# Kernel optimization log

Measured on AMD Instinct MI355X. Metric: run time of the kernel, lower is better.

Reference implementation:

```python
import jax, jax.numpy as jnp
import numpy as np

D_MODEL = 1024
H = 16
D_K = D_MODEL // H  # 64


def setup_inputs() -> dict:
    key = jax.random.key(0)
    ks = jax.random.split(key, 10)
    s = 1.0 / np.sqrt(D_MODEL)
    x = jax.random.normal(ks[0], (4, 2048, D_MODEL), dtype=jnp.float32)
    # Per-head linear weights stacked: [H, d_model, d_k]
    Wq = jax.random.uniform(ks[1], (H, D_MODEL, D_K), jnp.float32, -s, s)
    bq = jax.random.uniform(ks[2], (H, D_K), jnp.float32, -s, s)
    Wk = jax.random.uniform(ks[3], (H, D_MODEL, D_K), jnp.float32, -s, s)
    bk = jax.random.uniform(ks[4], (H, D_K), jnp.float32, -s, s)
    Wv = jax.random.uniform(ks[5], (H, D_MODEL, D_K), jnp.float32, -s, s)
    bv = jax.random.uniform(ks[6], (H, D_K), jnp.float32, -s, s)
    so = 1.0 / np.sqrt(H * D_K)
    Wo = jax.random.uniform(ks[7], (H * D_K, D_MODEL), jnp.float32, -so, so)
    bo = jax.random.uniform(ks[8], (D_MODEL,), jnp.float32, -so, so)
    return {"x": x, "Wq": Wq, "bq": bq, "Wk": Wk, "bk": bk, "Wv": Wv, "bv": bv, "Wo": Wo, "bo": bo}


def reference(x, Wq, bq, Wk, bk, Wv, bv, Wo, bo):
    # x: [B, S, D]; Wq/Wk/Wv: [H, D, d_k]; b*: [H, d_k]
    q = jnp.einsum('bsd,hdk->bhsk', x, Wq) + bq[None, :, None, :]
    k = jnp.einsum('bsd,hdk->bhsk', x, Wk) + bk[None, :, None, :]
    v = jnp.einsum('bsd,hdk->bhsk', x, Wv) + bv[None, :, None, :]
    scores = jnp.einsum('bhqk,bhsk->bhqs', q, k) / np.sqrt(D_K)
    S = x.shape[1]
    causal = jnp.triu(jnp.ones((S, S), dtype=bool), k=1)  # True above diagonal
    scores = jnp.where(causal, -jnp.inf, scores)
    attn = jax.nn.softmax(scores, axis=-1)
    ctx = jnp.einsum('bhqs,bhsk->bhqk', attn, v)  # [B, H, S, d_k]
    B = x.shape[0]
    # concat heads: torch cats head outputs along last dim -> [B, S, H*d_k]
    ctx = jnp.transpose(ctx, (0, 2, 1, 3)).reshape(B, S, H * D_K)
    return ctx @ Wo + bo
```

## Files before the change

kernel.cpp:

```cpp
#include <hip/hip_runtime.h>
#include <hip/hip_bf16.h>

typedef unsigned short u16;
typedef __attribute__((ext_vector_type(8))) short short8;
typedef __attribute__((ext_vector_type(4))) short short4v;
typedef __attribute__((ext_vector_type(4))) float floatx4;

#define D_MODEL 1024
#define NH 16
#define SEQ 2048
#define BATCH 4
#define M_ROWS 8192
#define N_QKV 3072
#define PS_LD 72

#define QSCALE 0.18033688011112042f
#define EXP2_OFF 11.541560327111707f

__device__ __forceinline__ u16 f2u(float f) {
    __hip_bfloat16 h = __float2bfloat16(f);
    u16 u; __builtin_memcpy(&u, &h, 2); return u;
}

__device__ __forceinline__ void async_copy16(const u16* g, u16* l) {
    __builtin_amdgcn_global_load_lds(
        (const __attribute__((address_space(1))) unsigned int*)(g),
        (__attribute__((address_space(3))) unsigned int*)(l),
        16, 0, 0);
}

__global__ __launch_bounds__(256) void prep(
    const float* __restrict__ x,
    const float* __restrict__ Wq, const float* __restrict__ Wk,
    const float* __restrict__ Wv, const float* __restrict__ Wo,
    const float* __restrict__ bq, const float* __restrict__ bk,
    const float* __restrict__ bv, const float* __restrict__ bo,
    u16* __restrict__ xb, u16* __restrict__ Wpt, u16* __restrict__ Wot,
    float* __restrict__ biasp)
{
    __shared__ u16 T[64 * 72];
    const int tid = threadIdx.x;
    const int blk = blockIdx.x;

    if (blk < 4096) {
        size_t i = ((size_t)blk * 256 + tid) * 8;
        float4 f0 = *(const float4*)&x[i];
        float4 f1 = *(const float4*)&x[i + 4];
        u16 t[8] = {f2u(f0.x), f2u(f0.y), f2u(f0.z), f2u(f0.w),
                    f2u(f1.x), f2u(f1.y), f2u(f1.z), f2u(f1.w)};
        *(short8*)&xb[i] = *(short8*)t;
        return;
    }
    if (blk == 5120) {
        #pragma unroll
        for (int j = 0; j < 16; j++) {
            int idx = j * 256 + tid;
            float v;
            if (idx < 1024)      v = bq[idx] * QSCALE;
            else if (idx < 2048) v = bk[idx - 1024];
            else if (idx < 3072) v = bv[idx - 2048];
            else                 v = bo[idx - 3072];
            biasp[idx] = v;
        }
        return;
    }
    const int wb = blk - 4096;
    const int r = tid >> 2, s4 = (tid & 3) * 16;
    if (wb < 768) {
        int sel = wb / 256, rem = wb % 256;
        int h = rem >> 4, ktile = rem & 15;
        const float* W = (sel == 0) ? Wq : ((sel == 1) ? Wk : Wv);
        const float scale = (sel == 0) ? QSCALE : 1.0f;
        const float* src = W + ((size_t)h * 1024 + ktile * 64 + r) * 64 + s4;
        #pragma unroll
        for (int i = 0; i < 16; i++) T[(s4 + i) * 72 + r] = f2u(src[i] * scale);
        __syncthreads();
        u16 tmp[16];
        #pragma unroll
        for (int i = 0; i < 16; i++) tmp[i] = T[r * 72 + s4 + i];
        u16* dst = Wpt + ((size_t)sel * 1024 + h * 64 + r) * 1024 + ktile * 64 + s4;
        *(short8*)&dst[0] = *(short8*)&tmp[0];
        *(short8*)&dst[8] = *(short8*)&tmp[8];
    } else {
        int rem = wb - 768;
        int nt = rem >> 4, kt2 = rem & 15;
        const float* src = Wo + ((size_t)kt2 * 64 + r) * 1024 + nt * 64 + s4;
        #pragma unroll
        for (int i = 0; i < 16; i++) T[(s4 + i) * 72 + r] = f2u(src[i]);
        __syncthreads();
        u16 tmp[16];
        #pragma unroll
        for (int i = 0; i < 16; i++) tmp[i] = T[r * 72 + s4 + i];
        u16* dst = Wot + ((size_t)nt * 64 + r) * 1024 + kt2 * 64 + s4;
        *(short8*)&dst[0] = *(short8*)&tmp[0];
        *(short8*)&dst[8] = *(short8*)&tmp[8];
    }
}

__global__ __launch_bounds__(256) void vtrans(const u16* __restrict__ QKV,
                                              u16* __restrict__ Vtg) {
    __shared__ u16 T[64 * 72];
    const int bh = blockIdx.x, kt = blockIdx.y;
    const int b = bh >> 4, h = bh & 15;
    const int tid = threadIdx.x;
    const int r = tid >> 2, s4 = (tid & 3) * 16;
    const u16* vp = QKV + (size_t)(b * SEQ + kt * 64 + r) * N_QKV + 2 * D_MODEL + h * 64 + s4;
    *(short8*)&T[r * 72 + s4]     = *(const short8*)&vp[0];
    *(short8*)&T[r * 72 + s4 + 8] = *(const short8*)&vp[8];
    __syncthreads();
    u16 tmp[16];
    #pragma unroll
    for (int i = 0; i < 16; i++) tmp[i] = T[(s4 + i) * 72 + r];
    u16* op = Vtg + ((size_t)bh * 64 + r) * SEQ + kt * 64 + s4;
    *(short8*)&op[0] = *(short8*)&tmp[0];
    *(short8*)&op[8] = *(short8*)&tmp[8];
}

template <typename OT>
__global__ __launch_bounds__(256) void gemm128(
    const u16* __restrict__ A, const u16* __restrict__ Bt,
    const float* __restrict__ bias, OT* __restrict__ C,
    int M, int N, int K)
{
    __shared__ u16 As[128 * 64];
    __shared__ u16 Bs[128 * 64];
    const int tid = threadIdx.x;
    const int w = tid >> 6, lane = tid & 63;
    const int l16 = lane & 15, quad = lane >> 4;

    const int nwgx = gridDim.x;
    const int nwg = nwgx * gridDim.y;
    const int lin = blockIdx.y * nwgx + blockIdx.x;
    const int cpx = nwg >> 3;
    const int swz = (lin & 7) * cpx + (lin >> 3);
    const int bn = (swz % nwgx) * 128, bm = (swz / nwgx) * 128;

    const int wr = (w >> 1) * 64, wc = (w & 1) * 64;

    floatx4 acc[4][4];
    #pragma unroll
    for (int i = 0; i < 4; i++)
        #pragma unroll
        for (int j = 0; j < 4; j++) acc[i][j] = (floatx4){0.f, 0.f, 0.f, 0.f};

    for (int k0 = 0; k0 < K; k0 += 64) {
        #pragma unroll
        for (int c = 0; c < 4; c++) {
            const int off = (w * 4 + c) * 1024 + lane * 16;
            const int row = off >> 7, seg = (off >> 4) & 7;
            async_copy16(A  + (size_t)(bm + row) * K + k0 + seg * 8, &As[(w * 4 + c) * 512]);
            async_copy16(Bt + (size_t)(bn + row) * K + k0 + seg * 8, &Bs[(w * 4 + c) * 512]);
        }
        __syncthreads();
        #pragma unroll
        for (int kc = 0; kc < 2; kc++) {
            short8 a[4], b[4];
            #pragma unroll
            for (int i = 0; i < 4; i++)
                a[i] = *(short8*)&As[(wr + i * 16 + l16) * 64 + kc * 32 + quad * 8];
            #pragma unroll
            for (int i = 0; i < 4; i++)
                b[i] = *(short8*)&Bs[(wc + i * 16 + l16) * 64 + kc * 32 + quad * 8];
            #pragma unroll
            for (int mm = 0; mm < 4; mm++)
                #pragma unroll
                for (int nn = 0; nn < 4; nn++)
                    acc[mm][nn] = __builtin_amdgcn_mfma_f32_16x16x32_bf16(
                        a[mm], b[nn], acc[mm][nn], 0, 0, 0);
        }
        __syncthreads();
    }

    #pragma unroll
    for (int nn = 0; nn < 4; nn++) {
        const int col = bn + wc + nn * 16 + l16;
        const float bi = bias[col];
        #pragma unroll
        for (int mm = 0; mm < 4; mm++) {
            const int row = bm + wr + mm * 16 + quad * 4;
            #pragma unroll
            for (int r = 0; r < 4; r++) {
                float v = acc[mm][nn][r] + bi;
                if constexpr (sizeof(OT) == 2) ((u16*)C)[(size_t)(row + r) * N + col] = f2u(v);
                else                           C[(size_t)(row + r) * N + col] = v;
            }
        }
    }
}

#define G256_BAR   __builtin_amdgcn_s_barrier()
#define G256_LGKM0 { asm volatile("s_waitcnt lgkmcnt(0)" ::: "memory"); \
                     __builtin_amdgcn_sched_barrier(0); }

#define G256_STG(dstbase, s0, s1) { \
    async_copy16((s0), &lds[(dstbase) + stw]); \
    async_copy16((s1), &lds[(dstbase) + 4096 + stw]); }

#define G256_STAGE_A(bb, half, kq) \
    G256_STG((bb) * 32768 + (half) * 8192, \
             pA[0] + (size_t)(half) * hstep + (kq), \
             pA[1] + (size_t)(half) * hstep + (kq))

#define G256_STAGE_B(bb, half, kq) \
    G256_STG((bb) * 32768 + 16384 + (half) * 8192, \
             pB[0] + (size_t)(half) * hstep + (kq), \
             pB[1] + (size_t)(half) * hstep + (kq))

#define G256_LDA4(dst, bb, mi0) { \
    const int _b = (bb) * 32768 + wm * 8192; \
    _Pragma("unroll") \
    for (int mi = 0; mi < 4; mi++) { \
        const int _r = _b + (((mi0) + mi) * 16 + l16) * 64; \
        dst[mi * 2]     = *(const short8*)&lds[_r + col0]; \
        dst[mi * 2 + 1] = *(const short8*)&lds[_r + col1]; \
    } }

#define G256_LDB2(dst, bb, ni0) { \
    const int _b = (bb) * 32768 + 16384 + (wn >> 1) * 8192 + (wn & 1) * 4096; \
    _Pragma("unroll") \
    for (int ni = 0; ni < 2; ni++) { \
        const int _r = _b + (((ni0) + ni) * 16 + l16) * 64; \
        dst[ni * 2]     = *(const short8*)&lds[_r + col0]; \
        dst[ni * 2 + 1] = *(const short8*)&lds[_r + col1]; \
    } }

#define G256_MMA8(av, bv, MI0, NI0) { \
    _Pragma("unroll") \
    for (int mi = 0; mi < 4; mi++) \
    _Pragma("unroll") \
    for (int ni = 0; ni < 2; ni++) { \
        acc[(MI0) + mi][(NI0) + ni] = __builtin_amdgcn_mfma_f32_16x16x32_bf16( \
            bv[ni * 2],     av[mi * 2],     acc[(MI0) + mi][(NI0) + ni], 0, 0, 0); \
        acc[(MI0) + mi][(NI0) + ni] = __builtin_amdgcn_mfma_f32_16x16x32_bf16( \
            bv[ni * 2 + 1], av[mi * 2 + 1], acc[(MI0) + mi][(NI0) + ni], 0, 0, 0); \
    } }

template <typename OT>
__global__ __launch_bounds__(512, 2) void gemm256(
    const u16* __restrict__ A, const u16* __restrict__ Bt,
    const float* __restrict__ bias, OT* __restrict__ C,
    int M, int N, int K)
{
    __shared__ u16 lds[65536];
    const int tid = threadIdx.x;
    const int w = tid >> 6, lane = tid & 63;
    const int l16 = lane & 15, quad = lane >> 4;
    const int wm = w >> 2, wn = w & 3;

    const int nwgx = gridDim.x;
    const int nwg = nwgx * gridDim.y;
    const int lin = blockIdx.y * nwgx + blockIdx.x;
    const int cpx = nwg >> 3;
    const int swz = (lin & 7) * cpx + (lin >> 3);
    const int bn = (swz % nwgx) * 256, bm = (swz / nwgx) * 256;

    const u16* pA[2]; const u16* pB[2];
    #pragma unroll
    for (int j = 0; j < 2; j++) {
        const int d = (j * 512 + tid) * 16;
        const int s = d ^ (((d >> 7) & 7) << 4);
        const int r = s >> 7;
        const int c = (s & 127) >> 1;
        pA[j] = A  + (size_t)(bm + r) * K + c;
        pB[j] = Bt + (size_t)(bn + r) * K + c;
    }
    const size_t hstep = (size_t)128 * K;
    const int stw = w * 512;

    const int xm = (l16 & 7) << 3;
    const int col0 = (quad * 8) ^ xm;
    const int col1 = (32 + quad * 8) ^ xm;

    floatx4 acc[8][4];
    #pragma unroll
    for (int i = 0; i < 8; i++)
        #pragma unroll
        for (int j = 0; j < 4; j++) acc[i][j] = (floatx4){0.f, 0.f, 0.f, 0.f};

    G256_STAGE_A(0, 0, 0);  G256_STAGE_A(0, 1, 0);
    G256_STAGE_B(0, 0, 0);  G256_STAGE_B(0, 1, 0);
    G256_STAGE_B(1, 0, 64); G256_STAGE_B(1, 1, 64);
    G256_STAGE_A(1, 0, 64);
    asm volatile("s_waitcnt vmcnt(6)" ::: "memory");
    __syncthreads();

    short8 aL[8], aH[8], bL[4], bH[4];
    const int NKT = K >> 6;
    for (int kt = 0; kt < NKT; ++kt) {
        const int buf = kt & 1, nb = buf ^ 1;
        const int kqA = (kt + 1) << 6, kqB = (kt + 2) << 6;
        const bool st1 = (kt + 1 < NKT), st2 = (kt + 2 < NKT);

        G256_LDA4(aL, buf, 0);
        G256_LDB2(bL, buf, 0);
        if (st1) { G256_STAGE_A(nb, 1, kqA); }
        asm volatile("s_waitcnt lgkmcnt(8)" ::: "memory");
        G256_BAR; G256_LGKM0;
        __builtin_amdgcn_s_setprio(1); G256_MMA8(aL, bL, 0, 0);
        __builtin_amdgcn_s_setprio(0); G256_BAR;

        G256_LDB2(bH, buf, 2);
        G256_BAR; G256_LGKM0;
        __builtin_amdgcn_s_setprio(1); G256_MMA8(aL, bH, 0, 2);
        __builtin_amdgcn_s_setprio(0); G256_BAR;

        G256_LDA4(aH, buf, 4);
        if (st2) { G256_STAGE_B(buf, 0, kqB); }
        G256_BAR; G256_LGKM0;
        __builtin_amdgcn_s_setprio(1); G256_MMA8(aH, bH, 4, 2);
        __builtin_amdgcn_s_setprio(0); G256_BAR;

        if (st2) { G256_STAGE_B(buf, 1, kqB); G256_STAGE_A(buf, 0, kqB); }
        __builtin_amdgcn_s_setprio(1); G256_MMA8(aH, bL, 4, 0);
        __builtin_amdgcn_s_setprio(0);
        __builtin_amdgcn_sched_barrier(0);
        if (st2)      { asm volatile("s_waitcnt vmcnt(6)" ::: "memory"); }
        else if (st1) { asm volatile("s_waitcnt vmcnt(0)" ::: "memory"); }
        G256_BAR;
    }

    float4 bi[4];
    #pragma unroll
    for (int ni = 0; ni < 4; ni++)
        bi[ni] = *(const float4*)&bias[bn + wn * 64 + ni * 16 + quad * 4];
    #pragma unroll
    for (int mi = 0; mi < 8; mi++) {
        const int row = bm + wm * 128 + mi * 16 + l16;
        #pragma unroll
        for (int ni = 0; ni < 4; ni++) {
            const int col = bn + wn * 64 + ni * 16 + quad * 4;
            const float v0 = acc[mi][ni][0] + bi[ni].x;
            const float v1 = acc[mi][ni][1] + bi[ni].y;
            const float v2 = acc[mi][ni][2] + bi[ni].z;
            const float v3 = acc[mi][ni][3] + bi[ni].w;
            if constexpr (sizeof(OT) == 2) {
                u16 o[4] = {f2u(v0), f2u(v1), f2u(v2), f2u(v3)};
                *(short4v*)&((u16*)C)[(size_t)row * N + col] = *(short4v*)o;
            } else {
                float4 fv = {v0, v1, v2, v3};
                *(float4*)&C[(size_t)row * N + col] = fv;
            }
        }
    }
}

__global__ __launch_bounds__(256) void attn_mfma(
    const u16* __restrict__ QKV, const u16* __restrict__ Vtg, u16* __restrict__ ctx)
{
    __shared__ u16 Ks[2][64 * 64];
    __shared__ u16 Vs[2][64 * 64];
    __shared__ u16 Ps[128 * PS_LD];

    const int bh = blockIdx.x;
    const int qt = (int)(gridDim.y - 1) - (int)blockIdx.y;
    const int b = bh >> 4, h = bh & 15;
    const int tid = threadIdx.x;
    const int w = tid >> 6, lane = tid & 63;
    const int l16 = lane & 15, quad = lane >> 4;

    const int r0 = tid >> 3,        c0 = tid & 7;
    const int r1 = (256 + tid) >> 3, c1 = tid & 7;
    const int sw0 = c0 ^ (r0 & 7), sw1 = c1 ^ (r1 & 7);

    short8 q[2][2];
    #pragma unroll
    for (int m = 0; m < 2; m++) {
        const u16* qp = QKV + (size_t)(b * SEQ + qt * 128 + w * 32 + m * 16 + l16) * N_QKV + h * 64;
        q[m][0] = *(const short8*)&qp[quad * 8];
        q[m][1] = *(const short8*)&qp[32 + quad * 8];
    }

    short8 ones8;
    #pragma unroll
    for (int i = 0; i < 8; i++) ones8[i] = (short)0x3F80;

    floatx4 O[2][4];
    floatx4 lsum[2];
    #pragma unroll
    for (int m = 0; m < 2; m++) {
        lsum[m] = (floatx4){0.f, 0.f, 0.f, 0.f};
        #pragma unroll
        for (int i = 0; i < 4; i++) O[m][i] = (floatx4){0.f, 0.f, 0.f, 0.f};
    }

    const int nkt = 2 * qt + 2;
    const int qrow_w_max = qt * 128 + w * 32 + 31;

    const size_t kbase = (size_t)(b * SEQ) * N_QKV + D_MODEL + h * 64;
    const size_t vbase = (size_t)bh * 64 * SEQ;

    const u16* kpa = QKV + kbase + (size_t)r0 * N_QKV + c0 * 8;
    const u16* kpb = QKV + kbase + (size_t)r1 * N_QKV + c1 * 8;
    const u16* vpa = Vtg + vbase + (size_t)r0 * SEQ + c0 * 8;
    const u16* vpb = Vtg + vbase + (size_t)r1 * SEQ + c1 * 8;

    {
        float4 ka = *(const float4*)kpa;
        float4 kb = *(const float4*)kpb;
        float4 va = *(const float4*)vpa;
        float4 vb = *(const float4*)vpb;
        *(float4*)&Ks[0][r0 * 64 + sw0 * 8] = ka;
        *(float4*)&Ks[0][r1 * 64 + sw1 * 8] = kb;
        *(float4*)&Vs[0][r0 * 64 + sw0 * 8] = va;
        *(float4*)&Vs[0][r1 * 64 + sw1 * 8] = vb;
    }
    kpa += (size_t)64 * N_QKV; kpb += (size_t)64 * N_QKV;
    vpa += 64; vpb += 64;
    __syncthreads();

    for (int kt = 0; kt < nkt; kt++) {
        const int buf = kt & 1;
        const bool pre = (kt + 1 < nkt);
        float4 ka, kb, va, vb;
        if (pre) {
            ka = *(const float4*)kpa;
            kb = *(const float4*)kpb;
            va = *(const float4*)vpa;
            vb = *(const float4*)vpb;
            kpa += (size_t)64 * N_QKV; kpb += (size_t)64 * N_QKV;
            vpa += 64; vpb += 64;
        }

        if (kt * 64 <= qrow_w_max) {
            short8 kf[4][2];
            #pragma unroll
            for (int ns = 0; ns < 4; ns++) {
                const int rr = ns * 16 + l16, rs = rr & 7;
                kf[ns][0] = *(short8*)&Ks[buf][rr * 64 + (quad ^ rs) * 8];
                kf[ns][1] = *(short8*)&Ks[buf][rr * 64 + ((4 + quad) ^ rs) * 8];
            }
            const bool needMask = (kt * 64 + 63 > qt * 128 + w * 32);

            #pragma unroll
            for (int m = 0; m < 2; m++) {
                floatx4 z[4];
                __builtin_amdgcn_s_setprio(1);
                #pragma unroll
                for (int ns = 0; ns < 4; ns++) {
                    floatx4 t = (floatx4){0.f, 0.f, 0.f, 0.f};
                    t = __builtin_amdgcn_mfma_f32_16x16x32_bf16(kf[ns][0], q[m][0], t, 0, 0, 0);
                    t = __builtin_amdgcn_mfma_f32_16x16x32_bf16(kf[ns][1], q[m][1], t, 0, 0, 0);
                    z[ns] = t;
                }
                __builtin_amdgcn_s_setprio(0);
                const int qrow_g = qt * 128 + w * 32 + m * 16 + l16;
                const int prow = (w * 32 + m * 16 + l16) * PS_LD;
                #pragma unroll
                for (int ns = 0; ns < 4; ns++) {
                    u16 pk[4];
                    #pragma unroll
                    for (int r = 0; r < 4; r++) {
                        float s = z[ns][r];
                        const int key = kt * 64 + ns * 16 + quad * 4 + r;
                        if (needMask && key > qrow_g) s = -INFINITY;
                        float p = __builtin_amdgcn_exp2f(s - EXP2_OFF);
                        pk[r] = f2u(p);
                    }
                    *(short4v*)&Ps[prow + ns * 16 + quad * 4] = *(short4v*)pk;
                }
            }

            short8 vf[4][2];
            #pragma unroll
            for (int ds = 0; ds < 4; ds++) {
                const int rr = ds * 16 + l16, rs = rr & 7;
                vf[ds][0] = *(short8*)&Vs[buf][rr * 64 + (quad ^ rs) * 8];
                vf[ds][1] = *(short8*)&Vs[buf][rr * 64 + ((4 + quad) ^ rs) * 8];
            }
            __builtin_amdgcn_s_setprio(1);
            #pragma unroll
            for (int m = 0; m < 2; m++) {
                const int prow = (w * 32 + m * 16 + l16) * PS_LD;
                short8 p0 = *(short8*)&Ps[prow + quad * 8];
                short8 p1 = *(short8*)&Ps[prow + 32 + quad * 8];
                lsum[m] = __builtin_amdgcn_mfma_f32_16x16x32_bf16(ones8, p0, lsum[m], 0, 0, 0);
                lsum[m] = __builtin_amdgcn_mfma_f32_16x16x32_bf16(ones8, p1, lsum[m], 0, 0, 0);
                #pragma unroll
                for (int ds = 0; ds < 4; ds++) {
                    O[m][ds] = __builtin_amdgcn_mfma_f32_16x16x32_bf16(vf[ds][0], p0, O[m][ds], 0, 0, 0);
                    O[m][ds] = __builtin_amdgcn_mfma_f32_16x16x32_bf16(vf[ds][1], p1, O[m][ds], 0, 0, 0);
                }
            }
            __builtin_amdgcn_s_setprio(0);
        }

        if (pre) {
            const int nb = buf ^ 1;
            *(float4*)&Ks[nb][r0 * 64 + sw0 * 8] = ka;
            *(float4*)&Ks[nb][r1 * 64 + sw1 * 8] = kb;
            *(float4*)&Vs[nb][r0 * 64 + sw0 * 8] = va;
            *(float4*)&Vs[nb][r1 * 64 + sw1 * 8] = vb;
        }
        __syncthreads();
    }

    #pragma unroll
    for (int m = 0; m < 2; m++) {
        const float inv = 1.0f / lsum[m][0];
        const size_t base = (size_t)(b * SEQ + qt * 128 + w * 32 + m * 16 + l16) * D_MODEL + h * 64;
        #pragma unroll
        for (int ds = 0; ds < 4; ds++) {
            u16 o[4];
            #pragma unroll
            for (int r = 0; r < 4; r++) o[r] = f2u(O[m][ds][r] * inv);
            *(short4v*)&ctx[base + ds * 16 + quad * 4] = *(short4v*)o;
        }
    }
}

extern "C" void kernel_launch(void* const* d_in, const int* in_sizes, int n_in,
                              void* d_out, int out_size, void* d_ws, size_t ws_size,
                              hipStream_t stream) {
    const float* x  = (const float*)d_in[0];
    const float* Wq = (const float*)d_in[1];
    const float* bq = (const float*)d_in[2];
    const float* Wk = (const float*)d_in[3];
    const float* bk = (const float*)d_in[4];
    const float* Wv = (const float*)d_in[5];
    const float* bv = (const float*)d_in[6];
    const float* Wo = (const float*)d_in[7];
    const float* bo = (const float*)d_in[8];
    float* out = (float*)d_out;

    char* ws = (char*)d_ws;
    float* biasp = (float*)ws;
    u16*   Wpt   = (u16*)(ws + 0x10000);
    u16*   Wot   = (u16*)(ws + 0x620000);
    u16*   xb    = (u16*)(ws + 0x840000);
    u16*   Vtg   = xb;
    u16*   QKV   = (u16*)(ws + 0x1840000);
    u16*   ctx   = (u16*)(ws + 0x4840000);

    prep<<<5121, 256, 0, stream>>>(x, Wq, Wk, Wv, Wo, bq, bk, bv, bo,
                                   xb, Wpt, Wot, biasp);

    gemm256<u16><<<dim3(N_QKV / 256, M_ROWS / 256), 512, 0, stream>>>(
        xb, Wpt, biasp, QKV, M_ROWS, N_QKV, D_MODEL);

    vtrans<<<dim3(64, 32), 256, 0, stream>>>(QKV, Vtg);

    attn_mfma<<<dim3(BATCH * NH, SEQ / 128), 256, 0, stream>>>(QKV, Vtg, ctx);

    gemm128<float><<<dim3(D_MODEL / 128, M_ROWS / 128), 256, 0, stream>>>(
        ctx, Wot, biasp + N_QKV, out, M_ROWS, D_MODEL, D_MODEL);
}
```

Baseline: 282.6 us.

## Prefetch next k-tile LDS fragments before the last MFMA block in GEMM loop

Restructures the 256-tile GEMM main loop so the A/B register fragments for the next k-tile are loaded from LDS while the final MFMA quadrant of the current tile runs. The ordering of MFMA quadrants changes and partial lgkmcnt waits replace full drains, so LDS reads overlap more with matrix math. This costs extra register pressure from holding the next tile's fragments early, and depends on the vmcnt/barrier ordering still being correct for buffer reuse.

```diff
diff --git a/kernel.cpp b/kernel.cpp
--- a/kernel.cpp
+++ b/kernel.cpp
@@ -189,8 +189,8 @@
 }
 
 #define G256_BAR   __builtin_amdgcn_s_barrier()
-#define G256_LGKM0 { asm volatile("s_waitcnt lgkmcnt(0)" ::: "memory"); \
-                     __builtin_amdgcn_sched_barrier(0); }
+#define G256_LGKM(n) { asm volatile("s_waitcnt lgkmcnt(" #n ")" ::: "memory"); \
+                       __builtin_amdgcn_sched_barrier(0); }
 
 #define G256_STG(dstbase, s0, s1) { \
     async_copy16((s0), &lds[(dstbase) + stw]); \
@@ -284,39 +284,43 @@
     asm volatile("s_waitcnt vmcnt(6)" ::: "memory");
     __syncthreads();
 
-    short8 aL[8], aH[8], bL[4], bH[4];
+    short8 a0[8], a1[8], b0[4], b1[4];
+    G256_LDA4(a0, 0, 0);
+    G256_LDB2(b0, 0, 0);
+
     const int NKT = K >> 6;
     for (int kt = 0; kt < NKT; ++kt) {
         const int buf = kt & 1, nb = buf ^ 1;
         const int kqA = (kt + 1) << 6, kqB = (kt + 2) << 6;
         const bool st1 = (kt + 1 < NKT), st2 = (kt + 2 < NKT);
 
-        G256_LDA4(aL, buf, 0);
-        G256_LDB2(bL, buf, 0);
+        G256_LDB2(b1, buf, 2);
         if (st1) { G256_STAGE_A(nb, 1, kqA); }
-        asm volatile("s_waitcnt lgkmcnt(8)" ::: "memory");
-        G256_BAR; G256_LGKM0;
-        __builtin_amdgcn_s_setprio(1); G256_MMA8(aL, bL, 0, 0);
+        G256_BAR; G256_LGKM(4);
+        __builtin_amdgcn_s_setprio(1); G256_MMA8(a0, b0, 0, 0);
         __builtin_amdgcn_s_setprio(0); G256_BAR;
 
-        G256_LDB2(bH, buf, 2);
-        G256_BAR; G256_LGKM0;
-        __builtin_amdgcn_s_setprio(1); G256_MMA8(aL, bH, 0, 2);
+        G256_LDA4(a1, buf, 4);
+        G256_BAR; G256_LGKM(8);
+        __builtin_amdgcn_s_setprio(1); G256_MMA8(a0, b1, 0, 2);
         __builtin_amdgcn_s_setprio(0); G256_BAR;
 
-        G256_LDA4(aH, buf, 4);
         if (st2) { G256_STAGE_B(buf, 0, kqB); }
-        G256_BAR; G256_LGKM0;
-        __builtin_amdgcn_s_setprio(1); G256_MMA8(aH, bH, 4, 2);
+        G256_BAR; G256_LGKM(0);
+        __builtin_amdgcn_s_setprio(1); G256_MMA8(a1, b0, 4, 0);
         __builtin_amdgcn_s_setprio(0); G256_BAR;
 
         if (st2) { G256_STAGE_B(buf, 1, kqB); G256_STAGE_A(buf, 0, kqB); }
-        __builtin_amdgcn_s_setprio(1); G256_MMA8(aH, bL, 4, 0);
-        __builtin_amdgcn_s_setprio(0);
-        __builtin_amdgcn_sched_barrier(0);
-        if (st2)      { asm volatile("s_waitcnt vmcnt(6)" ::: "memory"); }
-        else if (st1) { asm volatile("s_waitcnt vmcnt(0)" ::: "memory"); }
+        if (st1) {
+            if (st2) { asm volatile("s_waitcnt vmcnt(6)" ::: "memory"); }
+            else     { asm volatile("s_waitcnt vmcnt(0)" ::: "memory"); }
+            __builtin_amdgcn_sched_barrier(0);
+            G256_LDA4(a0, nb, 0);
+            G256_LDB2(b0, nb, 0);
+        }
         G256_BAR;
+        __builtin_amdgcn_s_setprio(1); G256_MMA8(a1, b1, 4, 2);
+        __builtin_amdgcn_s_setprio(0); G256_BAR;
     }
 
     float4 bi[4];
```

Measured after the change: 284.1 us. Within noise of the previous version (+0.5%).
